# Kernel tuning notes

Hardware: AMD Instinct MI355X
Metric: run time of the kernel (lower is better)

Reference implementation:

```python
import jax, jax.numpy as jnp
import numpy as np

PAD = 0
N_SENSE = 3
VOCAB = 100000
OUT_VOCAB = 50000
D = 128
B = 64
MAX_LEN = 512


def setup_inputs() -> dict:
    key = jax.random.key(0)
    ks = jax.random.split(key, 8)
    inputs = jax.random.randint(ks[0], (B, MAX_LEN * N_SENSE), 0, VOCAB, dtype=jnp.int64 if jax.config.jax_enable_x64 else jnp.int32)
    length_weights = jax.random.uniform(ks[1], (B, 1, 1), dtype=jnp.float32, minval=0.1, maxval=1.0)
    word_attn_mask = jax.random.bernoulli(ks[2], 0.1, (B, MAX_LEN))
    embedding = jax.random.normal(ks[3], (VOCAB, D), dtype=jnp.float32) * 0.02
    W_attn = jax.random.normal(ks[4], (1, D), dtype=jnp.float32) * 0.02
    b_attn = jnp.zeros((1,), dtype=jnp.float32)
    W_lin = jax.random.normal(ks[5], (OUT_VOCAB, D), dtype=jnp.float32) * 0.02
    b_lin = jnp.zeros((OUT_VOCAB,), dtype=jnp.float32)
    return {"inputs": inputs, "length_weights": length_weights, "word_attn_mask": word_attn_mask,
            "embedding": embedding, "W_attn": W_attn, "b_attn": b_attn, "W_lin": W_lin, "b_lin": b_lin}


def reference(inputs, length_weights, word_attn_mask, embedding, W_attn, b_attn, W_lin, b_lin):
    Bsz, LS = inputs.shape
    L = LS // N_SENSE
    # padding row contributes zeros (nn.Embedding padding_idx=PAD)
    E = embedding.at[PAD].set(0.0)
    embeds = E[inputs]                                   # [B, L*S, D]
    embeds4 = embeds.reshape(Bsz, L, N_SENSE, -1)
    embed_mean = embeds4.mean(axis=2)                    # [B, L, D]
    # word-level attention: Linear(D,1) -> mask -> softmax over words
    word_imp = jnp.einsum('bld,d->bl', embed_mean, W_attn[0]) + b_attn[0]
    word_imp = jnp.where(word_attn_mask, -jnp.inf, word_imp)
    word_w = jax.nn.softmax(word_imp, axis=-1)           # [B, L]
    context = jnp.einsum('bl,bld->bd', word_w, embed_mean)  # [B, D]
    # sense-level attention: similarity of each sense embedding to context
    sim = jnp.einsum('bnd,bd->bn', embeds, context)      # [B, L*S]
    sense_w = jax.nn.softmax(sim.reshape(Bsz, L, N_SENSE), axis=-1).reshape(Bsz, LS)
    attn_w = length_weights.reshape(Bsz, 1) * sense_w    # scale by 1/length
    attn_w = jnp.where(inputs == PAD, 0.0, attn_w)
    hidden = jnp.einsum('bn,bnd->bd', attn_w, embeds)    # [B, D]
    logits = hidden @ W_lin.T + b_lin                    # [B, OUT_VOCAB]
    return jax.nn.log_softmax(logits, axis=-1)
```

## Files before the change

kernel.cpp:

```cpp
#include <hip/hip_runtime.h>
#include <math.h>

#define B_    64
#define L_    512
#define S_    3
#define D_    128
#define OV_   50000
#define VOC_  100000
#define NBLK_ 782

typedef __attribute__((ext_vector_type(8))) short bf16x8;
typedef __attribute__((ext_vector_type(4))) float f32x4;

__device__ __forceinline__ float waveReduceSum(float v) {
#pragma unroll
    for (int off = 32; off >= 1; off >>= 1) v += __shfl_xor(v, off, 64);
    return v;
}
__device__ __forceinline__ float waveReduceMax(float v) {
#pragma unroll
    for (int off = 32; off >= 1; off >>= 1) v = fmaxf(v, __shfl_xor(v, off, 64));
    return v;
}

__device__ __forceinline__ short f2bf(float f) {
    unsigned int u = __float_as_uint(f);
    return (short)((u + 0x7FFFu + ((u >> 16) & 1u)) >> 16);
}

__global__ __launch_bounds__(256) void prequery_kernel(
    const float* __restrict__ emb, const float* __restrict__ Wa,
    float* __restrict__ P)
{
    const int lane = threadIdx.x & 63;
    const int q = lane >> 4;
    const int j = lane & 15;
    const int waveg = blockIdx.x * 4 + (threadIdx.x >> 6);
    const int nwaves = gridDim.x * 4;

    const float4 wa0 = ((const float4*)Wa)[2 * j];
    const float4 wa1 = ((const float4*)Wa)[2 * j + 1];

    for (int r0 = waveg * 4; r0 < VOC_; r0 += nwaves * 4) {
        const float4* row = (const float4*)(emb + (long)(r0 + q) * D_ + j * 8);
        float4 e0 = row[0], e1 = row[1];
        float s = e0.x * wa0.x + e0.y * wa0.y + e0.z * wa0.z + e0.w * wa0.w
                + e1.x * wa1.x + e1.y * wa1.y + e1.z * wa1.z + e1.w * wa1.w;
#pragma unroll
        for (int off = 8; off >= 1; off >>= 1) s += __shfl_xor(s, off, 64);
        if (j == 0) P[r0 + q] = s;
    }
}

__global__ __launch_bounds__(256) void wordsoftmax_kernel(
    const int* __restrict__ inputs, const int* __restrict__ mask,
    const float* __restrict__ P, const float* __restrict__ ba,
    float* __restrict__ wword, float* __restrict__ context,
    float* __restrict__ hidden)
{
    const int b   = blockIdx.x;
    const int tid = threadIdx.x;
    const int wave = tid >> 6, lane = tid & 63;

    if (tid < D_) { context[b * D_ + tid] = 0.f; hidden[b * D_ + tid] = 0.f; }

    __shared__ float s_imp[L_];
    __shared__ float s_red[4];

    const int* in_b = inputs + b * (L_ * S_);
    const float babias = ba[0];

#pragma unroll
    for (int half = 0; half < 2; ++half) {
        const int l = tid + half * 256;
        float acc = 0.f;
#pragma unroll
        for (int s = 0; s < S_; ++s) {
            int idx = in_b[l * S_ + s];
            if (idx != 0) acc += P[idx];
        }
        float imp = acc * (1.0f / 3.0f) + babias;
        s_imp[l] = mask[b * L_ + l] ? -INFINITY : imp;
    }
    __syncthreads();

    float v0 = s_imp[tid], v1 = s_imp[tid + 256];
    float m = waveReduceMax(fmaxf(v0, v1));
    if (lane == 0) s_red[wave] = m;
    __syncthreads();
    m = fmaxf(fmaxf(s_red[0], s_red[1]), fmaxf(s_red[2], s_red[3]));
    __syncthreads();
    float p0 = expf(v0 - m), p1 = expf(v1 - m);
    float ssum = waveReduceSum(p0 + p1);
    if (lane == 0) s_red[wave] = ssum;
    __syncthreads();
    float inv = 1.0f / (s_red[0] + s_red[1] + s_red[2] + s_red[3]);
    wword[b * L_ + tid]       = p0 * inv;
    wword[b * L_ + tid + 256] = p1 * inv;
}

__global__ __launch_bounds__(256) void context_kernel(
    const int* __restrict__ inputs, const float* __restrict__ wword,
    const float* __restrict__ emb, float* __restrict__ context)
{
    const int b    = blockIdx.x >> 4;
    const int base = (blockIdx.x & 15) * 32;
    const int tid  = threadIdx.x;
    const int wave = tid >> 6, lane = tid & 63;
    const int h = lane >> 5, j = lane & 31;

    __shared__ float s_w[32];
    __shared__ float s_part[8][D_];

    if (tid < 32) s_w[tid] = wword[b * L_ + base + tid] * (1.0f / 3.0f);
    __syncthreads();

    const int* in_b = inputs + b * (L_ * S_);
    float4 c = make_float4(0.f, 0.f, 0.f, 0.f);

    for (int wp = wave; wp < 16; wp += 4) {
        const int lw = wp * 2 + h;
        const int l  = base + lw;
        const float w = s_w[lw];
        float4 m = make_float4(0.f, 0.f, 0.f, 0.f);
#pragma unroll
        for (int s = 0; s < S_; ++s) {
            int idx = in_b[l * S_ + s];
            if (idx != 0) {
                float4 e = ((const float4*)(emb + (long)idx * D_))[j];
                m.x += e.x; m.y += e.y; m.z += e.z; m.w += e.w;
            }
        }
        c.x += w * m.x; c.y += w * m.y; c.z += w * m.z; c.w += w * m.w;
    }
    ((float4*)s_part[wave * 2 + h])[j] = c;
    __syncthreads();
    if (tid < D_) {
        float acc = 0.f;
#pragma unroll
        for (int p = 0; p < 8; ++p) acc += s_part[p][tid];
        atomicAdd(&context[b * D_ + tid], acc);
    }
}

__global__ __launch_bounds__(256) void sense_kernel(
    const int* __restrict__ inputs, const float* __restrict__ lwp,
    const float* __restrict__ context, const float* __restrict__ emb,
    float* __restrict__ hidden)
{
    const int b    = blockIdx.x >> 4;
    const int base = (blockIdx.x & 15) * 32;
    const int tid  = threadIdx.x;
    const int wave = tid >> 6, lane = tid & 63;
    const int h = lane >> 5, j = lane & 31;

    __shared__ float s_part[8][D_];

    const int* in_b = inputs + b * (L_ * S_);
    const float lwb = lwp[b];
    const float4 c4 = ((const float4*)(context + b * D_))[j];

    float4 hacc = make_float4(0.f, 0.f, 0.f, 0.f);

    for (int wp = wave; wp < 16; wp += 4) {
        const int l = base + wp * 2 + h;
        float4 e[S_]; int id[S_]; float sim[S_];
#pragma unroll
        for (int s = 0; s < S_; ++s) {
            id[s] = in_b[l * S_ + s];
            if (id[s] != 0) e[s] = ((const float4*)(emb + (long)id[s] * D_))[j];
            else e[s] = make_float4(0.f, 0.f, 0.f, 0.f);
            sim[s] = e[s].x * c4.x + e[s].y * c4.y + e[s].z * c4.z + e[s].w * c4.w;
        }
#pragma unroll
        for (int off = 16; off >= 1; off >>= 1) {
            sim[0] += __shfl_xor(sim[0], off, 64);
            sim[1] += __shfl_xor(sim[1], off, 64);
            sim[2] += __shfl_xor(sim[2], off, 64);
        }
        float mm = fmaxf(sim[0], fmaxf(sim[1], sim[2]));
        float e0 = expf(sim[0] - mm), e1 = expf(sim[1] - mm), e2 = expf(sim[2] - mm);
        float f = lwb / (e0 + e1 + e2);
        float w0 = (id[0] != 0) ? e0 * f : 0.f;
        float w1 = (id[1] != 0) ? e1 * f : 0.f;
        float w2 = (id[2] != 0) ? e2 * f : 0.f;
        hacc.x += w0 * e[0].x + w1 * e[1].x + w2 * e[2].x;
        hacc.y += w0 * e[0].y + w1 * e[1].y + w2 * e[2].y;
        hacc.z += w0 * e[0].z + w1 * e[1].z + w2 * e[2].z;
        hacc.w += w0 * e[0].w + w1 * e[1].w + w2 * e[2].w;
    }
    ((float4*)s_part[wave * 2 + h])[j] = hacc;
    __syncthreads();
    if (tid < D_) {
        float acc = 0.f;
#pragma unroll
        for (int p = 0; p < 8; ++p) acc += s_part[p][tid];
        atomicAdd(&hidden[b * D_ + tid], acc);
    }
}

__global__ __launch_bounds__(256) void logits_kernel(
    const float* __restrict__ hidden, const float* __restrict__ Wl,
    const float* __restrict__ bl, float* __restrict__ logits,
    float* __restrict__ pM, float* __restrict__ pS)
{
    const int tid  = threadIdx.x;
    const int wave = tid >> 6, lane = tid & 63;
    const int m15  = lane & 15, quad = lane >> 4;
    const int v    = blockIdx.x * 64 + wave * 16 + m15;
    const bool valid = (v < OV_);
    const int vc   = valid ? v : (OV_ - 1);

    bf16x8 afrag[4][4];
#pragma unroll
    for (int t = 0; t < 4; ++t) {
        const float* hrow = hidden + (t * 16 + m15) * D_ + quad * 8;
#pragma unroll
        for (int ks = 0; ks < 4; ++ks) {
            float4 x0 = *(const float4*)(hrow + ks * 32);
            float4 x1 = *(const float4*)(hrow + ks * 32 + 4);
            bf16x8 a;
            a[0] = f2bf(x0.x); a[1] = f2bf(x0.y); a[2] = f2bf(x0.z); a[3] = f2bf(x0.w);
            a[4] = f2bf(x1.x); a[5] = f2bf(x1.y); a[6] = f2bf(x1.z); a[7] = f2bf(x1.w);
            afrag[t][ks] = a;
        }
    }

    f32x4 acc[4];
#pragma unroll
    for (int t = 0; t < 4; ++t) acc[t] = (f32x4){0.f, 0.f, 0.f, 0.f};

    const float* wrow = Wl + (long)vc * D_ + quad * 8;
#pragma unroll
    for (int ks = 0; ks < 4; ++ks) {
        float4 x0 = *(const float4*)(wrow + ks * 32);
        float4 x1 = *(const float4*)(wrow + ks * 32 + 4);
        bf16x8 bfr;
        bfr[0] = f2bf(x0.x); bfr[1] = f2bf(x0.y); bfr[2] = f2bf(x0.z); bfr[3] = f2bf(x0.w);
        bfr[4] = f2bf(x1.x); bfr[5] = f2bf(x1.y); bfr[6] = f2bf(x1.z); bfr[7] = f2bf(x1.w);
#pragma unroll
        for (int t = 0; t < 4; ++t)
            acc[t] = __builtin_amdgcn_mfma_f32_16x16x32_bf16(afrag[t][ks], bfr,
                                                             acc[t], 0, 0, 0);
    }

    const float bias = bl[vc];
    if (valid) {
#pragma unroll
        for (int t = 0; t < 4; ++t)
#pragma unroll
            for (int r = 0; r < 4; ++r) {
                const int row = t * 16 + quad * 4 + r;
                logits[(long)row * OV_ + v] = acc[t][r] + bias;
            }
    }

    __shared__ float s_pm[64][4];
    __shared__ float s_ps[64][4];
#pragma unroll
    for (int t = 0; t < 4; ++t) {
#pragma unroll
        for (int r = 0; r < 4; ++r) {
            float x = valid ? acc[t][r] + bias : -INFINITY;
            float mx = x;
#pragma unroll
            for (int off = 8; off >= 1; off >>= 1)
                mx = fmaxf(mx, __shfl_xor(mx, off, 64));
            float se = valid ? expf(x - mx) : 0.f;
#pragma unroll
            for (int off = 8; off >= 1; off >>= 1) se += __shfl_xor(se, off, 64);
            if (m15 == 0) {
                const int row = t * 16 + quad * 4 + r;
                s_pm[row][wave] = mx;
                s_ps[row][wave] = se;
            }
        }
    }
    __syncthreads();
    if (tid < 64) {
        float m0 = s_pm[tid][0], m1 = s_pm[tid][1];
        float m2 = s_pm[tid][2], m3 = s_pm[tid][3];
        float m = fmaxf(fmaxf(m0, m1), fmaxf(m2, m3));
        float s = s_ps[tid][0] * expf(m0 - m) + s_ps[tid][1] * expf(m1 - m)
                + s_ps[tid][2] * expf(m2 - m) + s_ps[tid][3] * expf(m3 - m);
        pM[tid * NBLK_ + blockIdx.x] = m;
        pS[tid * NBLK_ + blockIdx.x] = s;
    }
}

__global__ __launch_bounds__(256) void reducez_kernel(
    const float* __restrict__ pM, const float* __restrict__ pS,
    float* __restrict__ logZ)
{
    const int b = blockIdx.x;
    const int tid = threadIdx.x;
    const int wave = tid >> 6, lane = tid & 63;
    const float* rm = pM + b * NBLK_;
    const float* rs = pS + b * NBLK_;
    __shared__ float s_red[4];

    float m = -INFINITY;
    for (int i = tid; i < NBLK_; i += 256) m = fmaxf(m, rm[i]);
    m = waveReduceMax(m);
    if (lane == 0) s_red[wave] = m;
    __syncthreads();
    m = fmaxf(fmaxf(s_red[0], s_red[1]), fmaxf(s_red[2], s_red[3]));
    __syncthreads();

    float s = 0.f;
    for (int i = tid; i < NBLK_; i += 256) s += rs[i] * expf(rm[i] - m);
    s = waveReduceSum(s);
    if (lane == 0) s_red[wave] = s;
    __syncthreads();
    if (tid == 0)
        logZ[b] = m + logf(s_red[0] + s_red[1] + s_red[2] + s_red[3]);
}

__global__ __launch_bounds__(256) void finalize_kernel(
    const float* __restrict__ logits, const float* __restrict__ logZ,
    float* __restrict__ out)
{
    const long i4 = (long)blockIdx.x * 256 + threadIdx.x;
    const long e  = i4 * 4;
    const int b = (int)(e / OV_);
    const float z = logZ[b];
    float4 x = ((const float4*)logits)[i4];
    x.x -= z; x.y -= z; x.z -= z; x.w -= z;
    ((float4*)out)[i4] = x;
}

extern "C" void kernel_launch(void* const* d_in, const int* in_sizes, int n_in,
                              void* d_out, int out_size, void* d_ws, size_t ws_size,
                              hipStream_t stream) {
    const int*   inputs = (const int*)d_in[0];
    const float* lw     = (const float*)d_in[1];
    const int*   mask   = (const int*)d_in[2];
    const float* emb    = (const float*)d_in[3];
    const float* Wa     = (const float*)d_in[4];
    const float* ba     = (const float*)d_in[5];
    const float* Wl     = (const float*)d_in[6];
    const float* bl     = (const float*)d_in[7];
    float* out = (float*)d_out;

    float* ws = (float*)d_ws;
    float* hidden  = ws;
    float* logZ    = ws + 8192;
    float* logits  = ws + 8256;
    float* P       = logits + (long)B_ * OV_;
    float* wword   = P + VOC_;
    float* context = wword + B_ * L_;
    float* pM      = context + B_ * D_;
    float* pS      = pM + B_ * NBLK_;

    prequery_kernel<<<625, 256, 0, stream>>>(emb, Wa, P);
    wordsoftmax_kernel<<<B_, 256, 0, stream>>>(inputs, mask, P, ba, wword,
                                               context, hidden);
    context_kernel<<<B_ * 16, 256, 0, stream>>>(inputs, wword, emb, context);
    sense_kernel<<<B_ * 16, 256, 0, stream>>>(inputs, lw, context, emb, hidden);
    logits_kernel<<<NBLK_, 256, 0, stream>>>(hidden, Wl, bl, logits, pM, pS);
    reducez_kernel<<<B_, 256, 0, stream>>>(pM, pS, logZ);
    finalize_kernel<<<(B_ * OV_) / (4 * 256), 256, 0, stream>>>(logits, logZ, out);
}
```

Measured before the change: 175.8 us.

## Fuse word softmax into context kernel and drop max-subtraction in softmaxes

Removes the separate word-softmax launch: each context block recomputes the full 512-word softmax for its batch row in shared memory, and the zeroing of context and hidden moves into the prequery kernel. The sense softmax and the log-softmax partials drop max subtraction, which removes the pM buffer and the shuffle-max passes. The logits kernel now stages hidden as bf16 in shared memory instead of holding A fragments in registers. The trade-off is 16x redundant softmax work per batch row and reliance on the logits and similarities staying small enough that exp cannot overflow, which holds only because the weights are small.

```diff
diff --git a/kernel.cpp b/kernel.cpp
--- a/kernel.cpp
+++ b/kernel.cpp
@@ -30,12 +30,19 @@
 
 __global__ __launch_bounds__(256) void prequery_kernel(
     const float* __restrict__ emb, const float* __restrict__ Wa,
-    float* __restrict__ P)
-{
-    const int lane = threadIdx.x & 63;
+    float* __restrict__ P, float* __restrict__ context,
+    float* __restrict__ hidden)
+{
+    const int tid = threadIdx.x;
+    if (blockIdx.x < 64 && tid < D_) {
+        context[blockIdx.x * D_ + tid] = 0.f;
+        hidden[blockIdx.x * D_ + tid]  = 0.f;
+    }
+
+    const int lane = tid & 63;
     const int q = lane >> 4;
     const int j = lane & 15;
-    const int waveg = blockIdx.x * 4 + (threadIdx.x >> 6);
+    const int waveg = blockIdx.x * 4 + (tid >> 6);
     const int nwaves = gridDim.x * 4;
 
     const float4 wa0 = ((const float4*)Wa)[2 * j];
@@ -52,55 +59,9 @@
     }
 }
 
-__global__ __launch_bounds__(256) void wordsoftmax_kernel(
+__global__ __launch_bounds__(256) void context_kernel(
     const int* __restrict__ inputs, const int* __restrict__ mask,
     const float* __restrict__ P, const float* __restrict__ ba,
-    float* __restrict__ wword, float* __restrict__ context,
-    float* __restrict__ hidden)
-{
-    const int b   = blockIdx.x;
-    const int tid = threadIdx.x;
-    const int wave = tid >> 6, lane = tid & 63;
-
-    if (tid < D_) { context[b * D_ + tid] = 0.f; hidden[b * D_ + tid] = 0.f; }
-
-    __shared__ float s_imp[L_];
-    __shared__ float s_red[4];
-
-    const int* in_b = inputs + b * (L_ * S_);
-    const float babias = ba[0];
-
-#pragma unroll
-    for (int half = 0; half < 2; ++half) {
-        const int l = tid + half * 256;
-        float acc = 0.f;
-#pragma unroll
-        for (int s = 0; s < S_; ++s) {
-            int idx = in_b[l * S_ + s];
-            if (idx != 0) acc += P[idx];
-        }
-        float imp = acc * (1.0f / 3.0f) + babias;
-        s_imp[l] = mask[b * L_ + l] ? -INFINITY : imp;
-    }
-    __syncthreads();
-
-    float v0 = s_imp[tid], v1 = s_imp[tid + 256];
-    float m = waveReduceMax(fmaxf(v0, v1));
-    if (lane == 0) s_red[wave] = m;
-    __syncthreads();
-    m = fmaxf(fmaxf(s_red[0], s_red[1]), fmaxf(s_red[2], s_red[3]));
-    __syncthreads();
-    float p0 = expf(v0 - m), p1 = expf(v1 - m);
-    float ssum = waveReduceSum(p0 + p1);
-    if (lane == 0) s_red[wave] = ssum;
-    __syncthreads();
-    float inv = 1.0f / (s_red[0] + s_red[1] + s_red[2] + s_red[3]);
-    wword[b * L_ + tid]       = p0 * inv;
-    wword[b * L_ + tid + 256] = p1 * inv;
-}
-
-__global__ __launch_bounds__(256) void context_kernel(
-    const int* __restrict__ inputs, const float* __restrict__ wword,
     const float* __restrict__ emb, float* __restrict__ context)
 {
     const int b    = blockIdx.x >> 4;
@@ -109,29 +70,56 @@
     const int wave = tid >> 6, lane = tid & 63;
     const int h = lane >> 5, j = lane & 31;
 
-    __shared__ float s_w[32];
+    __shared__ float s_imp[L_];
+    __shared__ float s_red[4];
     __shared__ float s_part[8][D_];
 
-    if (tid < 32) s_w[tid] = wword[b * L_ + base + tid] * (1.0f / 3.0f);
-    __syncthreads();
-
     const int* in_b = inputs + b * (L_ * S_);
+    const float babias = ba[0];
+
+#pragma unroll
+    for (int half = 0; half < 2; ++half) {
+        const int l = tid + half * 256;
+        float acc = 0.f;
+#pragma unroll
+        for (int s = 0; s < S_; ++s) {
+            int idx = in_b[l * S_ + s];
+            if (idx != 0) acc += P[idx];
+        }
+        float imp = acc * (1.0f / 3.0f) + babias;
+        s_imp[l] = mask[b * L_ + l] ? -INFINITY : imp;
+    }
+    __syncthreads();
+
+    float v0 = s_imp[tid], v1 = s_imp[tid + 256];
+    float m = waveReduceMax(fmaxf(v0, v1));
+    if (lane == 0) s_red[wave] = m;
+    __syncthreads();
+    m = fmaxf(fmaxf(s_red[0], s_red[1]), fmaxf(s_red[2], s_red[3]));
+    __syncthreads();
+    float p0 = expf(v0 - m), p1 = expf(v1 - m);
+    float ssum = waveReduceSum(p0 + p1);
+    if (lane == 0) s_red[wave] = ssum;
+    __syncthreads();
+    float inv = (1.0f / 3.0f) / (s_red[0] + s_red[1] + s_red[2] + s_red[3]);
+    s_imp[tid]       = p0 * inv;
+    s_imp[tid + 256] = p1 * inv;
+    __syncthreads();
+
     float4 c = make_float4(0.f, 0.f, 0.f, 0.f);
-
     for (int wp = wave; wp < 16; wp += 4) {
-        const int lw = wp * 2 + h;
-        const int l  = base + lw;
-        const float w = s_w[lw];
-        float4 m = make_float4(0.f, 0.f, 0.f, 0.f);
+        const int l = base + wp * 2 + h;
+        const float w = s_imp[l];
+        float4 mm = make_float4(0.f, 0.f, 0.f, 0.f);
 #pragma unroll
         for (int s = 0; s < S_; ++s) {
             int idx = in_b[l * S_ + s];
             if (idx != 0) {
                 float4 e = ((const float4*)(emb + (long)idx * D_))[j];
-                m.x += e.x; m.y += e.y; m.z += e.z; m.w += e.w;
+                mm.x += e.x; mm.y += e.y; mm.z += e.z; mm.w += e.w;
             }
         }
-        c.x += w * m.x; c.y += w * m.y; c.z += w * m.z; c.w += w * m.w;
+        c.x += w * mm.x; c.y += w * mm.y; c.z += w * mm.z; c.w += w * mm.w;
     }
     ((float4*)s_part[wave * 2 + h])[j] = c;
     __syncthreads();
@@ -178,8 +166,7 @@
             sim[1] += __shfl_xor(sim[1], off, 64);
             sim[2] += __shfl_xor(sim[2], off, 64);
         }
-        float mm = fmaxf(sim[0], fmaxf(sim[1], sim[2]));
-        float e0 = expf(sim[0] - mm), e1 = expf(sim[1] - mm), e2 = expf(sim[2] - mm);
+        float e0 = expf(sim[0]), e1 = expf(sim[1]), e2 = expf(sim[2]);
         float f = lwb / (e0 + e1 + e2);
         float w0 = (id[0] != 0) ? e0 * f : 0.f;
         float w1 = (id[1] != 0) ? e1 * f : 0.f;
@@ -202,8 +189,9 @@
 __global__ __launch_bounds__(256) void logits_kernel(
     const float* __restrict__ hidden, const float* __restrict__ Wl,
     const float* __restrict__ bl, float* __restrict__ logits,
-    float* __restrict__ pM, float* __restrict__ pS)
-{
+    float* __restrict__ pS)
+{
+    __shared__ short s_hbf[64][136];
     const int tid  = threadIdx.x;
     const int wave = tid >> 6, lane = tid & 63;
     const int m15  = lane & 15, quad = lane >> 4;
@@ -211,20 +199,15 @@
     const bool valid = (v < OV_);
     const int vc   = valid ? v : (OV_ - 1);
 
-    bf16x8 afrag[4][4];
-#pragma unroll
-    for (int t = 0; t < 4; ++t) {
-        const float* hrow = hidden + (t * 16 + m15) * D_ + quad * 8;
-#pragma unroll
-        for (int ks = 0; ks < 4; ++ks) {
-            float4 x0 = *(const float4*)(hrow + ks * 32);
-            float4 x1 = *(const float4*)(hrow + ks * 32 + 4);
-            bf16x8 a;
-            a[0] = f2bf(x0.x); a[1] = f2bf(x0.y); a[2] = f2bf(x0.z); a[3] = f2bf(x0.w);
-            a[4] = f2bf(x1.x); a[5] = f2bf(x1.y); a[6] = f2bf(x1.z); a[7] = f2bf(x1.w);
-            afrag[t][ks] = a;
-        }
-    }
+    for (int i = tid; i < 2048; i += 256) {
+        float4 x = ((const float4*)hidden)[i];
+        const int r = i >> 5;
+        const int c = (i & 31) * 4;
+        short* dst = &s_hbf[r][c];
+        dst[0] = f2bf(x.x); dst[1] = f2bf(x.y);
+        dst[2] = f2bf(x.z); dst[3] = f2bf(x.w);
+    }
+    __syncthreads();
 
     f32x4 acc[4];
 #pragma unroll
@@ -239,9 +222,11 @@
         bfr[0] = f2bf(x0.x); bfr[1] = f2bf(x0.y); bfr[2] = f2bf(x0.z); bfr[3] = f2bf(x0.w);
         bfr[4] = f2bf(x1.x); bfr[5] = f2bf(x1.y); bfr[6] = f2bf(x1.z); bfr[7] = f2bf(x1.w);
 #pragma unroll
-        for (int t = 0; t < 4; ++t)
-            acc[t] = __builtin_amdgcn_mfma_f32_16x16x32_bf16(afrag[t][ks], bfr,
+        for (int t = 0; t < 4; ++t) {
+            bf16x8 afr = *(const bf16x8*)&s_hbf[t * 16 + m15][ks * 32 + quad * 8];
+            acc[t] = __builtin_amdgcn_mfma_f32_16x16x32_bf16(afr, bfr,
                                                              acc[t], 0, 0, 0);
+        }
     }
 
     const float bias = bl[vc];
@@ -255,65 +240,39 @@
             }
     }
 
-    __shared__ float s_pm[64][4];
     __shared__ float s_ps[64][4];
 #pragma unroll
     for (int t = 0; t < 4; ++t) {
 #pragma unroll
         for (int r = 0; r < 4; ++r) {
-            float x = valid ? acc[t][r] + bias : -INFINITY;
-            float mx = x;
-#pragma unroll
-            for (int off = 8; off >= 1; off >>= 1)
-                mx = fmaxf(mx, __shfl_xor(mx, off, 64));
-            float se = valid ? expf(x - mx) : 0.f;
+            float se = valid ? expf(acc[t][r] + bias) : 0.f;
 #pragma unroll
             for (int off = 8; off >= 1; off >>= 1) se += __shfl_xor(se, off, 64);
-            if (m15 == 0) {
-                const int row = t * 16 + quad * 4 + r;
-                s_pm[row][wave] = mx;
-                s_ps[row][wave] = se;
-            }
-        }
-    }
-    __syncthreads();
-    if (tid < 64) {
-        float m0 = s_pm[tid][0], m1 = s_pm[tid][1];
-        float m2 = s_pm[tid][2], m3 = s_pm[tid][3];
-        float m = fmaxf(fmaxf(m0, m1), fmaxf(m2, m3));
-        float s = s_ps[tid][0] * expf(m0 - m) + s_ps[tid][1] * expf(m1 - m)
-                + s_ps[tid][2] * expf(m2 - m) + s_ps[tid][3] * expf(m3 - m);
-        pM[tid * NBLK_ + blockIdx.x] = m;
-        pS[tid * NBLK_ + blockIdx.x] = s;
-    }
+            if (m15 == 0) s_ps[t * 16 + quad * 4 + r][wave] = se;
+        }
+    }
+    __syncthreads();
+    if (tid < 64)
+        pS[tid * NBLK_ + blockIdx.x] = s_ps[tid][0] + s_ps[tid][1]
+                                     + s_ps[tid][2] + s_ps[tid][3];
 }
 
 __global__ __launch_bounds__(256) void reducez_kernel(
-    const float* __restrict__ pM, const float* __restrict__ pS,
-    float* __restrict__ logZ)
+    const float* __restrict__ pS, float* __restrict__ logZ)
 {
     const int b = blockIdx.x;
     const int tid = threadIdx.x;
     const int wave = tid >> 6, lane = tid & 63;
-    const float* rm = pM + b * NBLK_;
     const float* rs = pS + b * NBLK_;
     __shared__ float s_red[4];
 
-    float m = -INFINITY;
-    for (int i = tid; i < NBLK_; i += 256) m = fmaxf(m, rm[i]);
-    m = waveReduceMax(m);
-    if (lane == 0) s_red[wave] = m;
-    __syncthreads();
-    m = fmaxf(fmaxf(s_red[0], s_red[1]), fmaxf(s_red[2], s_red[3]));
-    __syncthreads();
-
     float s = 0.f;
-    for (int i = tid; i < NBLK_; i += 256) s += rs[i] * expf(rm[i] - m);
+    for (int i = tid; i < NBLK_; i += 256) s += rs[i];
     s = waveReduceSum(s);
     if (lane == 0) s_red[wave] = s;
     __syncthreads();
     if (tid == 0)
-        logZ[b] = m + logf(s_red[0] + s_red[1] + s_red[2] + s_red[3]);
+        logZ[b] = logf(s_red[0] + s_red[1] + s_red[2] + s_red[3]);
 }
 
 __global__ __launch_bounds__(256) void finalize_kernel(
@@ -347,17 +306,13 @@
     float* logZ    = ws + 8192;
     float* logits  = ws + 8256;
     float* P       = logits + (long)B_ * OV_;
-    float* wword   = P + VOC_;
-    float* context = wword + B_ * L_;
-    float* pM      = context + B_ * D_;
-    float* pS      = pM + B_ * NBLK_;
-
-    prequery_kernel<<<625, 256, 0, stream>>>(emb, Wa, P);
-    wordsoftmax_kernel<<<B_, 256, 0, stream>>>(inputs, mask, P, ba, wword,
-                                               context, hidden);
-    context_kernel<<<B_ * 16, 256, 0, stream>>>(inputs, wword, emb, context);
+    float* context = P + VOC_;
+    float* pS      = context + B_ * D_;
+
+    prequery_kernel<<<625, 256, 0, stream>>>(emb, Wa, P, context, hidden);
+    context_kernel<<<B_ * 16, 256, 0, stream>>>(inputs, mask, P, ba, emb, context);
     sense_kernel<<<B_ * 16, 256, 0, stream>>>(inputs, lw, context, emb, hidden);
-    logits_kernel<<<NBLK_, 256, 0, stream>>>(hidden, Wl, bl, logits, pM, pS);
-    reducez_kernel<<<B_, 256, 0, stream>>>(pM, pS, logZ);
+    logits_kernel<<<NBLK_, 256, 0, stream>>>(hidden, Wl, bl, logits, pS);
+    reducez_kernel<<<B_, 256, 0, stream>>>(pS, logZ);
     finalize_kernel<<<(B_ * OV_) / (4 * 256), 256, 0, stream>>>(logits, logZ, out);
 }
```

After: 161.0 us. -8.4%, faster.
